# Performance work log

Hardware: AMD Instinct MI355X
Metric: run time of the kernel (lower is better)

The kernel has to match this reference:

```python
import jax, jax.numpy as jnp
import numpy as np

B, N, DIM = 2, 2048, 1024
HEADS = 16
DIM_HEAD = DIM // HEADS  # 64
SCALE = DIM_HEAD ** -0.5


def setup_inputs() -> dict:
    key = jax.random.key(0)
    k1, k2, k3 = jax.random.split(key, 3)
    x = jax.random.normal(k1, (B, N, DIM), dtype=jnp.float32)
    W_qkv = jax.random.normal(k2, (DIM, 3 * HEADS * DIM_HEAD), dtype=jnp.float32) * (DIM ** -0.5)
    W_out = jax.random.normal(k3, (HEADS * DIM_HEAD, DIM), dtype=jnp.float32) * (DIM ** -0.5)
    return {"x": x, "W_qkv": W_qkv, "W_out": W_out}


def reference(x, W_qkv, W_out):
    b, n, _ = x.shape
    qkv = jnp.einsum('bnd,de->bne', x, W_qkv)  # [b, n, 3*h*dh]
    # faithful to einops 'b n (d k h) -> k b h n d': last axis factored as (dh, 3, h)
    qkv = qkv.reshape(b, n, DIM_HEAD, 3, HEADS)
    qkv = jnp.transpose(qkv, (3, 0, 4, 1, 2))  # [3, b, h, n, dh]
    q, k, v = qkv[0], qkv[1], qkv[2]
    scores = jnp.einsum('bhid,bhjd->bhij', q, k) * SCALE  # [b, h, n, n]
    causal_mask = jnp.triu(jnp.ones((n, n), dtype=bool), k=1)
    scores = jnp.where(causal_mask, -jnp.inf, scores)
    attn = jax.nn.softmax(scores, axis=-1)
    out = jnp.einsum('bhij,bhjd->bhid', attn, v)  # [b, h, n, dh]
    out = jnp.transpose(out, (0, 2, 1, 3)).reshape(b, n, HEADS * DIM_HEAD)  # 'b h n d -> b n (h d)'
    return jnp.einsum('bne,ed->bnd', out, W_out)
```

## Files before the change

kernel.cpp:

```cpp
#include <hip/hip_runtime.h>

typedef _Float16 f16;
typedef f16 half8 __attribute__((ext_vector_type(8)));
typedef f16 f16x4 __attribute__((ext_vector_type(4)));
typedef float f32x4 __attribute__((ext_vector_type(4)));

#define GLOAD_LDS16(gsrc, ldst)                                                              \
  __builtin_amdgcn_global_load_lds((const __attribute__((address_space(1))) void*)(gsrc),    \
                                   (__attribute__((address_space(3))) void*)(ldst), 16, 0, 0)

constexpr float SCALE = 0.125f;
constexpr float SCALE_L2E = 0.125f * 1.4426950408889634f;

static __device__ __forceinline__ f32x4 vmax4(f32x4 a, f32x4 b) {
  f32x4 r;
  r[0] = fmaxf(a[0], b[0]); r[1] = fmaxf(a[1], b[1]);
  r[2] = fmaxf(a[2], b[2]); r[3] = fmaxf(a[3], b[3]);
  return r;
}

__global__ __launch_bounds__(256) void k_cvt(const float4* __restrict__ in,
                                             f16x4* __restrict__ out, int n4) {
  int i = blockIdx.x * 256 + threadIdx.x;
  if (i < n4) {
    float4 v = in[i];
    f16x4 o;
    o[0] = (f16)v.x; o[1] = (f16)v.y; o[2] = (f16)v.z; o[3] = (f16)v.w;
    out[i] = o;
  }
}

__global__ __launch_bounds__(256) void k_transpose(const float* __restrict__ in,
                                                   f16* __restrict__ out, int R, int C) {
  __shared__ float t[32][33];
  int c0 = blockIdx.x * 32, r0 = blockIdx.y * 32;
  int tx = threadIdx.x, ty = threadIdx.y;
  for (int i = ty; i < 32; i += 8) t[i][tx] = in[(size_t)(r0 + i) * C + c0 + tx];
  __syncthreads();
  for (int i = ty; i < 32; i += 8) out[(size_t)(c0 + i) * R + r0 + tx] = (f16)t[tx][i];
}

__global__ __launch_bounds__(256) void k_transpose_qkv(const float* __restrict__ in,
                                                       f16* __restrict__ out) {
  __shared__ float t[32][33];
  int c0 = blockIdx.x * 32, r0 = blockIdx.y * 32;
  int tx = threadIdx.x, ty = threadIdx.y;
  for (int i = ty; i < 32; i += 8) t[i][tx] = in[(size_t)(r0 + i) * 3072 + c0 + tx];
  __syncthreads();
  for (int i = ty; i < 32; i += 8) {
    const int e = c0 + i;
    const int d = e / 48, rem = e - d * 48;
    const int k = rem >> 4, h = rem & 15;
    const int ep = k * 1024 + h * 64 + d;
    out[(size_t)ep * 1024 + r0 + tx] = (f16)t[tx][i];
  }
}

template <int MODE>
__global__ __launch_bounds__(256) void k_gemm(const f16* __restrict__ A,
                                              const f16* __restrict__ Bt,
                                              float* __restrict__ C,
                                              f16* __restrict__ Qp,
                                              f16* __restrict__ Kp,
                                              f16* __restrict__ Vt) {
  constexpr int K = 1024, BK = 64;
  __shared__ alignas(16) f16 smem[128 * 128];
  f16* As = smem;
  f16* Bs = smem + 128 * 64;
  const int tid = threadIdx.x;
  const int w = tid >> 6, lane = tid & 63;
  const int g = lane >> 4, lr = lane & 15;
  const int wr = w >> 1, wc = w & 1;
  const int m0 = blockIdx.y * 128, n0 = blockIdx.x * 128;
  const int srow = lane >> 3;
  const int scol = ((lane & 7) ^ srow) << 3;

  f32x4 acc[4][4] = {};

  for (int kt = 0; kt < K; kt += BK) {
    __syncthreads();
#pragma unroll
    for (int i = 0; i < 4; ++i) {
      const int chunk = w * 4 + i;
      const int row = chunk * 8 + srow;
      GLOAD_LDS16(A + (size_t)(m0 + row) * K + kt + scol, &As[chunk * 512]);
      GLOAD_LDS16(Bt + (size_t)(n0 + row) * K + kt + scol, &Bs[chunk * 512]);
    }
    __syncthreads();
#pragma unroll
    for (int c = 0; c < 2; ++c) {
      half8 af[4], bf[4];
#pragma unroll
      for (int m = 0; m < 4; ++m) {
        const int ra = wr * 64 + m * 16 + lr;
        const int off = ra * 128 + ((((c << 2) | g) ^ (ra & 7)) << 4);
        af[m] = *(const half8*)((const char*)As + off);
      }
#pragma unroll
      for (int n = 0; n < 4; ++n) {
        const int rb = wc * 64 + n * 16 + lr;
        const int off = rb * 128 + ((((c << 2) | g) ^ (rb & 7)) << 4);
        bf[n] = *(const half8*)((const char*)Bs + off);
      }
#pragma unroll
      for (int m = 0; m < 4; ++m)
#pragma unroll
        for (int n = 0; n < 4; ++n)
          acc[m][n] = __builtin_amdgcn_mfma_f32_16x16x32_f16(af[m], bf[n], acc[m][n], 0, 0, 0);
    }
  }

  if constexpr (MODE == 0) {
    const int sec = n0 >> 10;
    const int base = n0 & 1023;
    const int b = m0 >> 11;
    if (sec < 2) {
      f16* __restrict__ dst = (sec == 0) ? Qp : Kp;
      const float mul = (sec == 0) ? SCALE_L2E : 1.0f;
#pragma unroll
      for (int n = 0; n < 4; ++n) {
        const int idx = base + wc * 64 + n * 16 + lr;
        const int h = idx >> 6, d = idx & 63;
        f16* __restrict__ dh = dst + ((size_t)(b * 16 + h) * 2048) * 64 + d;
#pragma unroll
        for (int m = 0; m < 4; ++m)
#pragma unroll
          for (int r = 0; r < 4; ++r) {
            const int nn = (m0 & 2047) + wr * 64 + m * 16 + 4 * g + r;
            dh[(size_t)nn * 64] = (f16)(acc[m][n][r] * mul);
          }
      }
    } else {
      char* sb = (char*)smem;
      __syncthreads();
#pragma unroll
      for (int m = 0; m < 4; ++m)
#pragma unroll
        for (int n = 0; n < 4; ++n) {
          const int col = wc * 64 + n * 16 + lr;
          const int tok0 = wr * 64 + m * 16 + 4 * g;
          f16x4 v4;
#pragma unroll
          for (int r = 0; r < 4; ++r) v4[r] = (f16)acc[m][n][r];
          *(f16x4*)(sb + col * 256 + ((tok0 * 2) ^ ((col & 15) << 4))) = v4;
        }
      __syncthreads();
      const int nn0 = m0 & 2047;
#pragma unroll
      for (int pass = 0; pass < 8; ++pass) {
        const int c = w * 32 + pass * 4 + g;
        const int idx = base + c;
        const int h = idx >> 6, d = idx & 63;
        const half8 v = *(const half8*)(sb + c * 256 + ((lr * 16) ^ ((c & 15) << 4)));
        *(half8*)(Vt + ((size_t)(b * 16 + h) * 64 + d) * 2048 + nn0 + lr * 8) = v;
      }
    }
  } else {
#pragma unroll
    for (int m = 0; m < 4; ++m)
#pragma unroll
      for (int n = 0; n < 4; ++n)
#pragma unroll
        for (int r = 0; r < 4; ++r)
          C[(size_t)(m0 + wr * 64 + m * 16 + 4 * g + r) * 1024 +
            (n0 + wc * 64 + n * 16 + lr)] = acc[m][n][r];
  }
}

__global__ __launch_bounds__(64, 3) void k_attn(const f16* __restrict__ Q,
                                                const f16* __restrict__ Kp,
                                                const f16* __restrict__ Vt,
                                                f16* __restrict__ O) {
  __shared__ alignas(16) f16 plds[2][16][72];
  const int lane = threadIdx.x;
  const int g = lane >> 4, lr = lane & 15;
  const int id = (blockIdx.x & 7) * 256 + (blockIdx.x >> 3);
  const int bh = id >> 6;
  const int t = 63 - (id & 63);
  const int q0 = t * 32;

  const f16* __restrict__ Qb = Q + (size_t)bh * (2048 * 64);
  const f16* __restrict__ Kb = Kp + (size_t)bh * (2048 * 64);
  const f16* __restrict__ Vb = Vt + (size_t)bh * (64 * 2048);

  half8 qf[2][2];
#pragma unroll
  for (int f = 0; f < 2; ++f)
#pragma unroll
    for (int c = 0; c < 2; ++c)
      qf[f][c] = *(const half8*)(Qb + (size_t)(q0 + 16 * f + lr) * 64 + 32 * c + 8 * g);

  f32x4 acc[2][4] = {};
  float mrow[2] = {-INFINITY, -INFINITY};
  float lrow[2] = {0.f, 0.f};

  const int ntiles = (q0 >> 6) + 1;

  half8 kc[4][2], kn[4][2];
#pragma unroll
  for (int j = 0; j < 4; ++j)
#pragma unroll
    for (int c = 0; c < 2; ++c)
      kc[j][c] = *(const half8*)(Kb + (size_t)(16 * j + lr) * 64 + 32 * c + 8 * g);

  for (int kt = 0; kt < ntiles; ++kt) {
    const int k0 = kt * 64;
    const int knext = (kt + 1 < ntiles ? kt + 1 : kt) * 64;
#pragma unroll
    for (int j = 0; j < 4; ++j)
#pragma unroll
      for (int c = 0; c < 2; ++c)
        kn[j][c] = *(const half8*)(Kb + (size_t)(knext + 16 * j + lr) * 64 + 32 * c + 8 * g);

    __builtin_amdgcn_s_setprio(1);
    f32x4 st[2][4];
#pragma unroll
    for (int f = 0; f < 2; ++f)
#pragma unroll
      for (int j = 0; j < 4; ++j) {
        f32x4 z = {};
        z = __builtin_amdgcn_mfma_f32_16x16x32_f16(kc[j][0], qf[f][0], z, 0, 0, 0);
        st[f][j] = __builtin_amdgcn_mfma_f32_16x16x32_f16(kc[j][1], qf[f][1], z, 0, 0, 0);
      }
    __builtin_amdgcn_s_setprio(0);

    half8 va[4][2];
#pragma unroll
    for (int nb = 0; nb < 4; ++nb)
#pragma unroll
      for (int c = 0; c < 2; ++c)
        va[nb][c] = *(const half8*)(Vb + (size_t)(16 * nb + lr) * 2048 + k0 + 32 * c + 8 * g);

    if (k0 + 63 > q0) {
#pragma unroll
      for (int f = 0; f < 2; ++f)
#pragma unroll
        for (int j = 0; j < 4; ++j) {
          const int keyb = k0 + 16 * j + 4 * g;
          const int q = q0 + 16 * f + lr;
#pragma unroll
          for (int r = 0; r < 4; ++r)
            if (keyb + r > q) st[f][j][r] = -INFINITY;
        }
    }

    float sfv[2];
#pragma unroll
    for (int f = 0; f < 2; ++f) {
      f32x4 m4 = vmax4(vmax4(st[f][0], st[f][1]), vmax4(st[f][2], st[f][3]));
      float tm = fmaxf(fmaxf(m4[0], m4[1]), fmaxf(m4[2], m4[3]));
      tm = fmaxf(tm, __shfl_xor(tm, 16));
      tm = fmaxf(tm, __shfl_xor(tm, 32));
      const float mn = fmaxf(mrow[f], tm);
      sfv[f] = __builtin_amdgcn_exp2f(mrow[f] - mn);
      mrow[f] = mn;
#pragma unroll
      for (int j = 0; j < 4; ++j)
#pragma unroll
        for (int r = 0; r < 4; ++r)
          st[f][j][r] = __builtin_amdgcn_exp2f(st[f][j][r] - mn);
      f32x4 s4 = st[f][0] + st[f][1] + st[f][2] + st[f][3];
      float rs = (s4[0] + s4[1]) + (s4[2] + s4[3]);
      rs += __shfl_xor(rs, 16);
      rs += __shfl_xor(rs, 32);
      lrow[f] = lrow[f] * sfv[f] + rs;
#pragma unroll
      for (int j = 0; j < 4; ++j) {
        f16x4 v4;
#pragma unroll
        for (int r = 0; r < 4; ++r) v4[r] = (f16)st[f][j][r];
        *(f16x4*)(&plds[f][lr][16 * j + 4 * g]) = v4;
      }
    }

#pragma unroll
    for (int f = 0; f < 2; ++f)
#pragma unroll
      for (int r = 0; r < 4; ++r) {
        const float sb = __shfl(sfv[f], 4 * g + r);
#pragma unroll
        for (int nb = 0; nb < 4; ++nb) acc[f][nb][r] *= sb;
      }

    asm volatile("s_waitcnt lgkmcnt(0)" ::: "memory");
    __builtin_amdgcn_sched_barrier(0);
    half8 pf[2][2];
#pragma unroll
    for (int f = 0; f < 2; ++f)
#pragma unroll
      for (int c = 0; c < 2; ++c)
        pf[f][c] = *(const half8*)(&plds[f][lr][32 * c + 8 * g]);

    __builtin_amdgcn_s_setprio(1);
#pragma unroll
    for (int f = 0; f < 2; ++f)
#pragma unroll
      for (int nb = 0; nb < 4; ++nb) {
        acc[f][nb] = __builtin_amdgcn_mfma_f32_16x16x32_f16(pf[f][0], va[nb][0], acc[f][nb], 0, 0, 0);
        acc[f][nb] = __builtin_amdgcn_mfma_f32_16x16x32_f16(pf[f][1], va[nb][1], acc[f][nb], 0, 0, 0);
      }
    __builtin_amdgcn_s_setprio(0);
    __builtin_amdgcn_sched_barrier(0);

#pragma unroll
    for (int j = 0; j < 4; ++j)
#pragma unroll
      for (int c = 0; c < 2; ++c)
        kc[j][c] = kn[j][c];
  }

  const int b = bh >> 4, h = bh & 15;
#pragma unroll
  for (int f = 0; f < 2; ++f)
#pragma unroll
    for (int r = 0; r < 4; ++r) {
      const float lb = __shfl(lrow[f], 4 * g + r);
      const float inv = 1.f / lb;
      const int q = q0 + 16 * f + 4 * g + r;
      f16* orow = O + ((size_t)(b * 2048 + q) * 1024) + h * 64;
#pragma unroll
      for (int nb = 0; nb < 4; ++nb) orow[16 * nb + lr] = (f16)(acc[f][nb][r] * inv);
    }
}

extern "C" void kernel_launch(void* const* d_in, const int* in_sizes, int n_in,
                              void* d_out, int out_size, void* d_ws, size_t ws_size,
                              hipStream_t stream) {
  const float* x = (const float*)d_in[0];
  const float* Wqkv = (const float*)d_in[1];
  const float* Wout = (const float*)d_in[2];

  char* p = (char*)d_ws;
  f16* Xb = (f16*)p;    p += (size_t)4096 * 1024 * 2;
  f16* Wqkvt = (f16*)p; p += (size_t)3072 * 1024 * 2;
  f16* Woutt = (f16*)p; p += (size_t)1024 * 1024 * 2;
  f16* Qp = (f16*)p;    p += (size_t)32 * 2048 * 64 * 2;
  f16* Kp = (f16*)p;    p += (size_t)32 * 2048 * 64 * 2;
  f16* Vt = (f16*)p;    p += (size_t)32 * 64 * 2048 * 2;
  f16* O = (f16*)p;     p += (size_t)4096 * 1024 * 2;

  k_cvt<<<4096, 256, 0, stream>>>((const float4*)x, (f16x4*)Xb, 4096 * 1024 / 4);
  k_transpose_qkv<<<dim3(96, 32), dim3(32, 8), 0, stream>>>(Wqkv, Wqkvt);
  k_transpose<<<dim3(32, 32), dim3(32, 8), 0, stream>>>(Wout, Woutt, 1024, 1024);
  k_gemm<0><<<dim3(24, 32), 256, 0, stream>>>(Xb, Wqkvt, nullptr, Qp, Kp, Vt);
  k_attn<<<2048, 64, 0, stream>>>(Qp, Kp, Vt, O);
  k_gemm<1><<<dim3(8, 32), 256, 0, stream>>>(O, Woutt, (float*)d_out, nullptr, nullptr, nullptr);
}
```

Baseline: 252.2 us.

## Pair query tiles per attention block and stage output through LDS

```diff
diff --git a/kernel.cpp b/kernel.cpp
--- a/kernel.cpp
+++ b/kernel.cpp
@@ -12,11 +12,8 @@
 constexpr float SCALE = 0.125f;
 constexpr float SCALE_L2E = 0.125f * 1.4426950408889634f;
 
-static __device__ __forceinline__ f32x4 vmax4(f32x4 a, f32x4 b) {
-  f32x4 r;
-  r[0] = fmaxf(a[0], b[0]); r[1] = fmaxf(a[1], b[1]);
-  r[2] = fmaxf(a[2], b[2]); r[3] = fmaxf(a[3], b[3]);
-  return r;
+static __device__ __forceinline__ unsigned pk2(float a, float b) {
+  return __builtin_bit_cast(unsigned, __builtin_amdgcn_cvt_pkrtz(a, b));
 }
 
 __global__ __launch_bounds__(256) void k_cvt(const float4* __restrict__ in,
@@ -167,17 +164,19 @@
   }
 }
 
-__global__ __launch_bounds__(64, 3) void k_attn(const f16* __restrict__ Q,
-                                                const f16* __restrict__ Kp,
-                                                const f16* __restrict__ Vt,
-                                                f16* __restrict__ O) {
-  __shared__ alignas(16) f16 plds[2][16][72];
-  const int lane = threadIdx.x;
+__global__ __launch_bounds__(128, 3) void k_attn(const f16* __restrict__ Q,
+                                                 const f16* __restrict__ Kp,
+                                                 const f16* __restrict__ Vt,
+                                                 f16* __restrict__ O) {
+  __shared__ alignas(16) char plds_all[2][4608];
+  const int tid = threadIdx.x;
+  const int w = tid >> 6, lane = tid & 63;
   const int g = lane >> 4, lr = lane & 15;
-  const int id = (blockIdx.x & 7) * 256 + (blockIdx.x >> 3);
-  const int bh = id >> 6;
-  const int t = 63 - (id & 63);
-  const int q0 = t * 32;
+  const int gb = blockIdx.x;
+  const int j = 31 - (gb >> 5);
+  const int bh = gb & 31;
+  const int q0 = (2 * j + w) * 32;
+  char* pl = plds_all[w];
 
   const f16* __restrict__ Qb = Q + (size_t)bh * (2048 * 64);
   const f16* __restrict__ Kb = Kp + (size_t)bh * (2048 * 64);
@@ -194,33 +193,24 @@
   float mrow[2] = {-INFINITY, -INFINITY};
   float lrow[2] = {0.f, 0.f};
 
-  const int ntiles = (q0 >> 6) + 1;
-
-  half8 kc[4][2], kn[4][2];
-#pragma unroll
-  for (int j = 0; j < 4; ++j)
-#pragma unroll
-    for (int c = 0; c < 2; ++c)
-      kc[j][c] = *(const half8*)(Kb + (size_t)(16 * j + lr) * 64 + 32 * c + 8 * g);
-
-  for (int kt = 0; kt < ntiles; ++kt) {
+  for (int kt = 0; kt <= j; ++kt) {
     const int k0 = kt * 64;
-    const int knext = (kt + 1 < ntiles ? kt + 1 : kt) * 64;
-#pragma unroll
-    for (int j = 0; j < 4; ++j)
+    half8 kf[4][2];
+#pragma unroll
+    for (int jj = 0; jj < 4; ++jj)
 #pragma unroll
       for (int c = 0; c < 2; ++c)
-        kn[j][c] = *(const half8*)(Kb + (size_t)(knext + 16 * j + lr) * 64 + 32 * c + 8 * g);
+        kf[jj][c] = *(const half8*)(Kb + (size_t)(k0 + 16 * jj + lr) * 64 + 32 * c + 8 * g);
 
     __builtin_amdgcn_s_setprio(1);
     f32x4 st[2][4];
 #pragma unroll
     for (int f = 0; f < 2; ++f)
 #pragma unroll
-      for (int j = 0; j < 4; ++j) {
+      for (int jj = 0; jj < 4; ++jj) {
         f32x4 z = {};
-        z = __builtin_amdgcn_mfma_f32_16x16x32_f16(kc[j][0], qf[f][0], z, 0, 0, 0);
-        st[f][j] = __builtin_amdgcn_mfma_f32_16x16x32_f16(kc[j][1], qf[f][1], z, 0, 0, 0);
+        z = __builtin_amdgcn_mfma_f32_16x16x32_f16(kf[jj][0], qf[f][0], z, 0, 0, 0);
+        st[f][jj] = __builtin_amdgcn_mfma_f32_16x16x32_f16(kf[jj][1], qf[f][1], z, 0, 0, 0);
       }
     __builtin_amdgcn_s_setprio(0);
 
@@ -235,52 +225,50 @@
 #pragma unroll
       for (int f = 0; f < 2; ++f)
 #pragma unroll
-        for (int j = 0; j < 4; ++j) {
-          const int keyb = k0 + 16 * j + 4 * g;
+        for (int jj = 0; jj < 4; ++jj) {
+          const int keyb = k0 + 16 * jj + 4 * g;
           const int q = q0 + 16 * f + lr;
 #pragma unroll
           for (int r = 0; r < 4; ++r)
-            if (keyb + r > q) st[f][j][r] = -INFINITY;
+            if (keyb + r > q) st[f][jj][r] = -INFINITY;
         }
     }
 
     float sfv[2];
 #pragma unroll
     for (int f = 0; f < 2; ++f) {
-      f32x4 m4 = vmax4(vmax4(st[f][0], st[f][1]), vmax4(st[f][2], st[f][3]));
+      f32x4 m4 = st[f][0];
+#pragma unroll
+      for (int jj = 1; jj < 4; ++jj)
+#pragma unroll
+        for (int r = 0; r < 4; ++r) m4[r] = fmaxf(m4[r], st[f][jj][r]);
       float tm = fmaxf(fmaxf(m4[0], m4[1]), fmaxf(m4[2], m4[3]));
       tm = fmaxf(tm, __shfl_xor(tm, 16));
       tm = fmaxf(tm, __shfl_xor(tm, 32));
       const float mn = fmaxf(mrow[f], tm);
       sfv[f] = __builtin_amdgcn_exp2f(mrow[f] - mn);
       mrow[f] = mn;
-#pragma unroll
-      for (int j = 0; j < 4; ++j)
-#pragma unroll
-        for (int r = 0; r < 4; ++r)
-          st[f][j][r] = __builtin_amdgcn_exp2f(st[f][j][r] - mn);
-      f32x4 s4 = st[f][0] + st[f][1] + st[f][2] + st[f][3];
+      f32x4 s4 = {};
+#pragma unroll
+      for (int jj = 0; jj < 4; ++jj) {
+#pragma unroll
+        for (int r = 0; r < 4; ++r) {
+          st[f][jj][r] = __builtin_amdgcn_exp2f(st[f][jj][r] - mn);
+          s4[r] += st[f][jj][r];
+        }
+        const int rb = (16 * f + lr) * 144 + 32 * jj + 8 * g;
+        *(unsigned*)(pl + rb) = pk2(st[f][jj][0], st[f][jj][1]);
+        *(unsigned*)(pl + rb + 4) = pk2(st[f][jj][2], st[f][jj][3]);
+      }
       float rs = (s4[0] + s4[1]) + (s4[2] + s4[3]);
       rs += __shfl_xor(rs, 16);
       rs += __shfl_xor(rs, 32);
       lrow[f] = lrow[f] * sfv[f] + rs;
 #pragma unroll
-      for (int j = 0; j < 4; ++j) {
-        f16x4 v4;
-#pragma unroll
-        for (int r = 0; r < 4; ++r) v4[r] = (f16)st[f][j][r];
-        *(f16x4*)(&plds[f][lr][16 * j + 4 * g]) = v4;
-      }
-    }
-
-#pragma unroll
-    for (int f = 0; f < 2; ++f)
-#pragma unroll
-      for (int r = 0; r < 4; ++r) {
-        const float sb = __shfl(sfv[f], 4 * g + r);
-#pragma unroll
-        for (int nb = 0; nb < 4; ++nb) acc[f][nb][r] *= sb;
-      }
+      for (int nb = 0; nb < 4; ++nb)
+#pragma unroll
+        for (int r = 0; r < 4; ++r) acc[f][nb][r] *= sfv[f];
+    }
 
     asm volatile("s_waitcnt lgkmcnt(0)" ::: "memory");
     __builtin_amdgcn_sched_barrier(0);
@@ -289,38 +277,40 @@
     for (int f = 0; f < 2; ++f)
 #pragma unroll
       for (int c = 0; c < 2; ++c)
-        pf[f][c] = *(const half8*)(&plds[f][lr][32 * c + 8 * g]);
+        pf[f][c] = *(const half8*)(pl + (16 * f + lr) * 144 + 64 * c + 16 * g);
 
     __builtin_amdgcn_s_setprio(1);
 #pragma unroll
     for (int f = 0; f < 2; ++f)
 #pragma unroll
       for (int nb = 0; nb < 4; ++nb) {
-        acc[f][nb] = __builtin_amdgcn_mfma_f32_16x16x32_f16(pf[f][0], va[nb][0], acc[f][nb], 0, 0, 0);
-        acc[f][nb] = __builtin_amdgcn_mfma_f32_16x16x32_f16(pf[f][1], va[nb][1], acc[f][nb], 0, 0, 0);
+        acc[f][nb] = __builtin_amdgcn_mfma_f32_16x16x32_f16(va[nb][0], pf[f][0], acc[f][nb], 0, 0, 0);
+        acc[f][nb] = __builtin_amdgcn_mfma_f32_16x16x32_f16(va[nb][1], pf[f][1], acc[f][nb], 0, 0, 0);
       }
     __builtin_amdgcn_s_setprio(0);
     __builtin_amdgcn_sched_barrier(0);
-
-#pragma unroll
-    for (int j = 0; j < 4; ++j)
-#pragma unroll
-      for (int c = 0; c < 2; ++c)
-        kc[j][c] = kn[j][c];
-  }
-
+  }
+
+#pragma unroll
+  for (int f = 0; f < 2; ++f) {
+    const float inv = 1.f / lrow[f];
+#pragma unroll
+    for (int nb = 0; nb < 4; ++nb) {
+      const int rb = (16 * f + lr) * 144 + 32 * nb + 8 * g;
+      *(unsigned*)(pl + rb) = pk2(acc[f][nb][0] * inv, acc[f][nb][1] * inv);
+      *(unsigned*)(pl + rb + 4) = pk2(acc[f][nb][2] * inv, acc[f][nb][3] * inv);
+    }
+  }
+  asm volatile("s_waitcnt lgkmcnt(0)" ::: "memory");
+  __builtin_amdgcn_sched_barrier(0);
   const int b = bh >> 4, h = bh & 15;
-#pragma unroll
-  for (int f = 0; f < 2; ++f)
-#pragma unroll
-    for (int r = 0; r < 4; ++r) {
-      const float lb = __shfl(lrow[f], 4 * g + r);
-      const float inv = 1.f / lb;
-      const int q = q0 + 16 * f + 4 * g + r;
-      f16* orow = O + ((size_t)(b * 2048 + q) * 1024) + h * 64;
-#pragma unroll
-      for (int nb = 0; nb < 4; ++nb) orow[16 * nb + lr] = (f16)(acc[f][nb][r] * inv);
-    }
+  const int row = lane >> 1, half = lane & 1;
+  f16* orow = O + ((size_t)(b * 2048 + q0 + row) * 1024) + h * 64 + 32 * half;
+#pragma unroll
+  for (int k = 0; k < 4; ++k) {
+    const half8 v = *(const half8*)(pl + row * 144 + 64 * half + 16 * k);
+    *(half8*)(orow + 8 * k) = v;
+  }
 }
 
 extern "C" void kernel_launch(void* const* d_in, const int* in_sizes, int n_in,
@@ -343,6 +333,6 @@
   k_transpose_qkv<<<dim3(96, 32), dim3(32, 8), 0, stream>>>(Wqkv, Wqkvt);
   k_transpose<<<dim3(32, 32), dim3(32, 8), 0, stream>>>(Wout, Woutt, 1024, 1024);
   k_gemm<0><<<dim3(24, 32), 256, 0, stream>>>(Xb, Wqkvt, nullptr, Qp, Kp, Vt);
-  k_attn<<<2048, 64, 0, stream>>>(Qp, Kp, Vt, O);
+  k_attn<<<1024, 128, 0, stream>>>(Qp, Kp, Vt, O);
   k_gemm<1><<<dim3(8, 32), 256, 0, stream>>>(O, Woutt, (float*)d_out, nullptr, nullptr, nullptr);
 }
```

Result: faster. 229.3 us (-9.1%).
